# Performance work log

Hardware: AMD Instinct MI355X
Metric: run time of the kernel (lower is better)

The kernel has to match this reference:

```python
import jax, jax.numpy as jnp
import numpy as np

NUM_EMBEDDINGS = 1024
EMBEDDING_DIM = 256
COMMITMENT_COST = 0.25


def setup_inputs() -> dict:
    key = jax.random.key(0)
    k1, k2 = jax.random.split(key)
    inputs = jax.random.normal(k1, (32, EMBEDDING_DIM, 32, 32), dtype=jnp.float32)
    # torch init: uniform_(-1/K, 1/K)
    emb_w = jax.random.uniform(k2, (NUM_EMBEDDINGS, EMBEDDING_DIM), dtype=jnp.float32,
                               minval=-1.0 / NUM_EMBEDDINGS, maxval=1.0 / NUM_EMBEDDINGS)
    return {"inputs": inputs, "emb_w": emb_w}


def reference(inputs, emb_w):
    sg = jax.lax.stop_gradient
    # BCHW -> BHWC
    x = jnp.transpose(inputs, (0, 2, 3, 1))
    in_shape = x.shape
    flat = x.reshape(-1, EMBEDDING_DIM)  # [N, D]
    # squared L2 distances to codebook: [N, K]
    distances = (jnp.sum(flat * flat, axis=1, keepdims=True)
                 + jnp.sum(emb_w * emb_w, axis=1)
                 - 2.0 * jnp.matmul(flat, emb_w.T))
    idx = jnp.argmin(distances, axis=1)  # [N]
    encodings = jax.nn.one_hot(idx, NUM_EMBEDDINGS, dtype=jnp.float32)  # [N, K]
    # one-hot @ codebook == gather
    quantized = jnp.take(emb_w, idx, axis=0).reshape(in_shape)  # [B,H,W,D]
    e_latent_loss = jnp.mean((sg(quantized) - x) ** 2)
    q_latent_loss = jnp.mean((quantized - sg(x)) ** 2)
    loss = q_latent_loss + COMMITMENT_COST * e_latent_loss
    # straight-through estimator
    quantized_st = x + sg(quantized - x)
    avg_probs = jnp.mean(encodings, axis=0)
    perplexity = jnp.exp(-jnp.sum(avg_probs * jnp.log(avg_probs + 1e-10)))
    return (loss, jnp.transpose(quantized_st, (0, 3, 1, 2)), perplexity, encodings)
```

## Files before the change

kernel.cpp:

```cpp
#include <hip/hip_runtime.h>
#include <hip/hip_bf16.h>

typedef short short8 __attribute__((ext_vector_type(8)));
typedef float f32x4 __attribute__((ext_vector_type(4)));
typedef unsigned short u16x4 __attribute__((ext_vector_type(4)));

#define D_ 256
#define K_ 1024
#define HW_ 1024
#define NROWS_ 32768
#define QELEMS 8388608
#define NBLK_ (NROWS_ / 64)

static __device__ __forceinline__ unsigned short to_bf16(float v) {
    __hip_bfloat16 h = __float2bfloat16(v);
    return *(unsigned short*)&h;
}

__global__ __launch_bounds__(256) void vq_prep(const float* __restrict__ emb,
    unsigned short* __restrict__ ebf, float* __restrict__ enorm,
    int* __restrict__ counts, double* __restrict__ loss_acc, int* __restrict__ done)
{
    int k = blockIdx.x, t = threadIdx.x;
    float v = emb[k * D_ + t];
    ebf[k * D_ + t] = to_bf16(v);
    float s = v * v;
    for (int o = 32; o > 0; o >>= 1) s += __shfl_down(s, o);
    __shared__ float ws4[4];
    if ((t & 63) == 0) ws4[t >> 6] = s;
    __syncthreads();
    if (t == 0) enorm[k] = ws4[0] + ws4[1] + ws4[2] + ws4[3];
    if (k < 4) counts[k * 256 + t] = 0;
    if (k == 0 && t == 0) { *loss_acc = 0.0; *done = 0; }
}

__global__ __launch_bounds__(512, 4) void vq_main(
    const float* __restrict__ x, const float* __restrict__ emb,
    const unsigned short* __restrict__ ebf, const float* __restrict__ enorm,
    int* __restrict__ counts, double* __restrict__ loss_acc, int* __restrict__ done,
    float* __restrict__ out)
{
    __shared__ char smem[66560];
    __shared__ float xn[64][33];
    __shared__ float rminv[64][4];
    __shared__ int   rmini[64][4];
    __shared__ int   bestsh[64];
    __shared__ double sred2[8];
    __shared__ int lastflag;

    unsigned short* xs = (unsigned short*)smem;
    char* es = smem;

    const int t = threadIdx.x;
    const int n0 = blockIdx.x * 64;
    const int b = n0 >> 10;
    const int hw0 = n0 & 1023;
    const float* xbase = x + (size_t)b * (D_ * HW_) + hw0;

    {
        const int rt = t & 15;
        const int dg = t >> 4;
        const int r0 = rt * 4;
        float xp[4] = {0.f, 0.f, 0.f, 0.f};
#pragma unroll
        for (int m = 0; m < 2; ++m) {
            int d0 = (dg + 32 * m) * 4;
            f32x4 c[4];
#pragma unroll
            for (int q = 0; q < 4; ++q)
                c[q] = *(const f32x4*)(xbase + (size_t)(d0 + q) * HW_ + r0);
#pragma unroll
            for (int i = 0; i < 4; ++i) {
                u16x4 pk;
                pk[0] = to_bf16(c[0][i]); pk[1] = to_bf16(c[1][i]);
                pk[2] = to_bf16(c[2][i]); pk[3] = to_bf16(c[3][i]);
                xp[i] = fmaf(c[0][i], c[0][i], xp[i]);
                xp[i] = fmaf(c[1][i], c[1][i], xp[i]);
                xp[i] = fmaf(c[2][i], c[2][i], xp[i]);
                xp[i] = fmaf(c[3][i], c[3][i], xp[i]);
                int r = r0 + i;
                int byte = (r * 512 + d0 * 2) ^ ((r & 7) << 4);
                *(u16x4*)((char*)xs + byte) = pk;
            }
        }
#pragma unroll
        for (int i = 0; i < 4; ++i) xn[r0 + i][dg] = xp[i];
    }
    __syncthreads();

    const int lane = t & 63;
    const int w = t >> 6;
    const int rh = w & 1;
    const int cq = w >> 1;
    const int col = lane & 15;
    const int kg = lane >> 4;
    const char* ebf_bytes = (const char*)ebf;
    const int wbyte = w * 4096;

    {
#pragma unroll
        for (int j = 0; j < 4; ++j) {
            int p = wbyte + j * 1024 + lane * 16;
            int qq = p ^ (((p >> 9) & 7) << 4);
            __builtin_amdgcn_global_load_lds(ebf_bytes + qq, es + 32768 + wbyte + j * 1024, 16, 0, 0);
        }
    }

    short8 areg[2][8];
#pragma unroll
    for (int rt = 0; rt < 2; ++rt) {
        int row = rh * 32 + rt * 16 + col;
        int rowb = row * 512;
        int sw = (row & 7) << 4;
#pragma unroll
        for (int dc = 0; dc < 8; ++dc) {
            int byte = (rowb + dc * 64 + kg * 16) ^ sw;
            areg[rt][dc] = *(const short8*)((const char*)xs + byte);
        }
    }

    float v1[8]; int i1[8];
#pragma unroll
    for (int s = 0; s < 8; ++s) { v1[s] = 3.4e38f; i1[s] = 0x7fffffff; }

    float2* ezw = (float2*)(out + 8388610 + (size_t)(n0 + w * 8) * 1024);
    const float2 zz2 = {0.f, 0.f};

    for (int cc = 0; cc < 16; ++cc) {
        __syncthreads();
        const int hc = ((cc & 1) ^ 1) * 32768;
        if (cc < 15) {
            const char* src = ebf_bytes + (size_t)(cc + 1) * 32768;
            const int hn = (cc & 1) * 32768;
#pragma unroll
            for (int j = 0; j < 4; ++j) {
                int p = wbyte + j * 1024 + lane * 16;
                int qq = p ^ (((p >> 9) & 7) << 4);
                __builtin_amdgcn_global_load_lds(src + qq, es + hn + wbyte + j * 1024, 16, 0, 0);
            }
        }
        {
            float2* ez = ezw + cc * 256;
#pragma unroll
            for (int j = 0; j < 4; ++j) ez[j * 64 + lane] = zz2;
        }
        const int c0 = cq * 16 + col;
        const int sw0 = (c0 & 7) << 4;
        f32x4 acc0 = {0.f, 0.f, 0.f, 0.f};
        f32x4 acc1 = {0.f, 0.f, 0.f, 0.f};
#pragma unroll
        for (int dc = 0; dc < 8; ++dc) {
            short8 bf = *(const short8*)(es + hc + ((c0 * 512 + dc * 64 + kg * 16) ^ sw0));
            acc0 = __builtin_amdgcn_mfma_f32_16x16x32_bf16(areg[0][dc], bf, acc0, 0, 0, 0);
            acc1 = __builtin_amdgcn_mfma_f32_16x16x32_bf16(areg[1][dc], bf, acc1, 0, 0, 0);
        }
        int code = cc * 64 + c0;
        float bn = enorm[code];
#pragma unroll
        for (int r = 0; r < 4; ++r) {
            float dv = fmaf(-2.f, acc0[r], bn);
            if (dv < v1[r]) { v1[r] = dv; i1[r] = code; }
            float dw = fmaf(-2.f, acc1[r], bn);
            if (dw < v1[4 + r]) { v1[4 + r] = dw; i1[4 + r] = code; }
        }
    }

#pragma unroll
    for (int mask = 1; mask < 16; mask <<= 1) {
#pragma unroll
        for (int s = 0; s < 8; ++s) {
            float ov = __shfl_xor(v1[s], mask);
            int oi = __shfl_xor(i1[s], mask);
            if (ov < v1[s] || (ov == v1[s] && oi < i1[s])) { v1[s] = ov; i1[s] = oi; }
        }
    }
    if (col == 0) {
#pragma unroll
        for (int s = 0; s < 8; ++s) {
            int rt = s >> 2, r = s & 3;
            int row = rh * 32 + rt * 16 + kg * 4 + r;
            rminv[row][cq] = v1[s];
            rmini[row][cq] = i1[s];
        }
    }
    __syncthreads();

    if (t < 64) {
        float dmin = rminv[t][0]; int best = rmini[t][0];
#pragma unroll
        for (int g = 1; g < 4; ++g) {
            float cv = rminv[t][g]; int ci = rmini[t][g];
            if (cv < dmin || (cv == dmin && ci < best)) { dmin = cv; best = ci; }
        }
        bestsh[t] = best;
        atomicAdd(&counts[best], 1);
        float s = 0.f;
#pragma unroll 8
        for (int g = 0; g < 32; ++g) s += xn[t][g];
        float lrow = dmin + s;
        for (int o = 32; o > 0; o >>= 1) lrow += __shfl_down(lrow, o);
        if (t == 0) atomicAdd(loss_acc, (double)lrow);
    }
    __syncthreads();

    {
        int r = w * 8 + (lane & 7);
        int c = lane >> 3;
        const f32x4* src4 = (const f32x4*)emb + (size_t)bestsh[r] * 64 + c * 8;
        f32x4* dst4 = (f32x4*)smem + r * 65 + c * 8;
#pragma unroll
        for (int j = 0; j < 8; ++j) dst4[j] = src4[j];
    }
    __syncthreads();

    {
        const int hwr = t & 63;
        const int dq = t >> 6;
        float* outq = out + 1 + (size_t)b * (D_ * HW_) + hw0 + hwr;
        const float* qrow = (const float*)smem + hwr * 260;
#pragma unroll
        for (int dd = 0; dd < 32; ++dd) {
            int d = dq + dd * 8;
            outq[(size_t)d * HW_] = qrow[d];
        }
    }
    if (t < 64) out[8388610 + (size_t)(n0 + t) * 1024 + bestsh[t]] = 1.0f;
    __syncthreads();

    if (t == 0) {
        __threadfence();
        int old = atomicAdd(done, 1);
        lastflag = (old == NBLK_ - 1) ? 1 : 0;
    }
    __syncthreads();
    if (lastflag) {
        double s = 0.0;
#pragma unroll
        for (int j = 0; j < 2; ++j) {
            int k = t * 2 + j;
            int cnt = __hip_atomic_load(&counts[k], __ATOMIC_RELAXED, __HIP_MEMORY_SCOPE_AGENT);
            double p = (double)cnt / 32768.0;
            s += p * log(p + 1e-10);
        }
        for (int o = 32; o > 0; o >>= 1) s += __shfl_down(s, o);
        if (lane == 0) sred2[w] = s;
        __syncthreads();
        if (t == 0) {
            double tot = 0.0;
#pragma unroll
            for (int g = 0; g < 8; ++g) tot += sred2[g];
            double lw = __hip_atomic_load(loss_acc, __ATOMIC_RELAXED, __HIP_MEMORY_SCOPE_AGENT);
            out[0] = (float)(1.25 * lw / (double)QELEMS);
            out[8388609] = (float)exp(-tot);
        }
    }
}

extern "C" void kernel_launch(void* const* d_in, const int* in_sizes, int n_in,
                              void* d_out, int out_size, void* d_ws, size_t ws_size,
                              hipStream_t stream)
{
    const float* x = (const float*)d_in[0];
    const float* emb = (const float*)d_in[1];
    char* ws = (char*)d_ws;
    unsigned short* ebf = (unsigned short*)(ws);
    float* enorm = (float*)(ws + 524288);
    int* counts = (int*)(ws + 528384);
    double* lacc = (double*)(ws + 532480);
    int* done = (int*)(ws + 532488);
    float* out = (float*)d_out;

    vq_prep<<<K_, 256, 0, stream>>>(emb, ebf, enorm, counts, lacc, done);
    vq_main<<<NBLK_, 512, 0, stream>>>(x, emb, ebf, enorm, counts, lacc, done, out);
}
```

Baseline: 76.73 us.

## Cut LDS footprint, stage codebook norms in LDS, relax loop barrier waits

Shrinks shared memory by pre-reducing the per-row x-norm partials with shuffles (xn shrinks from 33 to 9 columns) and by swapping the padded quantized staging buffer for an XOR-swizzled one. This lets more blocks fit per CU under the 4-block launch bound. Codebook norms are copied once into LDS instead of being read from global memory on every chunk. The per-chunk __syncthreads is replaced by a partial vmcnt wait plus s_barrier, so the one-hot zero-fill stores can stay in flight, and the last chunk's zero stores are hoisted ahead of the loop. The vmcnt(4) count assumes a particular ordering of outstanding global loads and stores, which risks being subtly wrong.

```diff
diff --git a/kernel.cpp b/kernel.cpp
--- a/kernel.cpp
+++ b/kernel.cpp
@@ -40,8 +40,9 @@
     int* __restrict__ counts, double* __restrict__ loss_acc, int* __restrict__ done,
     float* __restrict__ out)
 {
-    __shared__ char smem[66560];
-    __shared__ float xn[64][33];
+    __shared__ char smem[65536];
+    __shared__ float xn[64][9];
+    __shared__ float ens[1024];
     __shared__ float rminv[64][4];
     __shared__ int   rmini[64][4];
     __shared__ int   bestsh[64];
@@ -57,10 +58,13 @@
     const int hw0 = n0 & 1023;
     const float* xbase = x + (size_t)b * (D_ * HW_) + hw0;
 
+    ens[t] = enorm[t];
+    ens[t + 512] = enorm[t + 512];
+
     {
         const int rt = t & 15;
+        const int r0 = rt * 4;
         const int dg = t >> 4;
-        const int r0 = rt * 4;
         float xp[4] = {0.f, 0.f, 0.f, 0.f};
 #pragma unroll
         for (int m = 0; m < 2; ++m) {
@@ -84,7 +88,15 @@
             }
         }
 #pragma unroll
-        for (int i = 0; i < 4; ++i) xn[r0 + i][dg] = xp[i];
+        for (int i = 0; i < 4; ++i) {
+            xp[i] += __shfl_down(xp[i], 32);
+            xp[i] += __shfl_down(xp[i], 16);
+        }
+        if ((t & 48) == 0) {
+            int w0 = t >> 6;
+#pragma unroll
+            for (int i = 0; i < 4; ++i) xn[r0 + i][w0] = xp[i];
+        }
     }
     __syncthreads();
 
@@ -97,6 +109,9 @@
     const char* ebf_bytes = (const char*)ebf;
     const int wbyte = w * 4096;
 
+    float2* ezw = (float2*)(out + 8388610 + (size_t)(n0 + w * 8) * 1024);
+    const float2 zz2 = {0.f, 0.f};
+
     {
 #pragma unroll
         for (int j = 0; j < 4; ++j) {
@@ -104,6 +119,11 @@
             int qq = p ^ (((p >> 9) & 7) << 4);
             __builtin_amdgcn_global_load_lds(ebf_bytes + qq, es + 32768 + wbyte + j * 1024, 16, 0, 0);
         }
+        __builtin_amdgcn_sched_barrier(0);
+        float2* ez = ezw + 15 * 256;
+#pragma unroll
+        for (int j = 0; j < 4; ++j) ez[j * 64 + lane] = zz2;
+        __builtin_amdgcn_sched_barrier(0);
     }
 
     short8 areg[2][8];
@@ -123,11 +143,10 @@
 #pragma unroll
     for (int s = 0; s < 8; ++s) { v1[s] = 3.4e38f; i1[s] = 0x7fffffff; }
 
-    float2* ezw = (float2*)(out + 8388610 + (size_t)(n0 + w * 8) * 1024);
-    const float2 zz2 = {0.f, 0.f};
-
     for (int cc = 0; cc < 16; ++cc) {
-        __syncthreads();
+        asm volatile("s_waitcnt vmcnt(4)" ::: "memory");
+        __builtin_amdgcn_s_barrier();
+        __builtin_amdgcn_sched_barrier(0);
         const int hc = ((cc & 1) ^ 1) * 32768;
         if (cc < 15) {
             const char* src = ebf_bytes + (size_t)(cc + 1) * 32768;
@@ -138,11 +157,11 @@
                 int qq = p ^ (((p >> 9) & 7) << 4);
                 __builtin_amdgcn_global_load_lds(src + qq, es + hn + wbyte + j * 1024, 16, 0, 0);
             }
-        }
-        {
+            __builtin_amdgcn_sched_barrier(0);
             float2* ez = ezw + cc * 256;
 #pragma unroll
             for (int j = 0; j < 4; ++j) ez[j * 64 + lane] = zz2;
+            __builtin_amdgcn_sched_barrier(0);
         }
         const int c0 = cq * 16 + col;
         const int sw0 = (c0 & 7) << 4;
@@ -155,7 +174,7 @@
             acc1 = __builtin_amdgcn_mfma_f32_16x16x32_bf16(areg[1][dc], bf, acc1, 0, 0, 0);
         }
         int code = cc * 64 + c0;
-        float bn = enorm[code];
+        float bn = ens[code];
 #pragma unroll
         for (int r = 0; r < 4; ++r) {
             float dv = fmaf(-2.f, acc0[r], bn);
@@ -195,8 +214,8 @@
         bestsh[t] = best;
         atomicAdd(&counts[best], 1);
         float s = 0.f;
-#pragma unroll 8
-        for (int g = 0; g < 32; ++g) s += xn[t][g];
+#pragma unroll
+        for (int g = 0; g < 8; ++g) s += xn[t][g];
         float lrow = dmin + s;
         for (int o = 32; o > 0; o >>= 1) lrow += __shfl_down(lrow, o);
         if (t == 0) atomicAdd(loss_acc, (double)lrow);
@@ -204,12 +223,21 @@
     __syncthreads();
 
     {
-        int r = w * 8 + (lane & 7);
-        int c = lane >> 3;
-        const f32x4* src4 = (const f32x4*)emb + (size_t)bestsh[r] * 64 + c * 8;
-        f32x4* dst4 = (f32x4*)smem + r * 65 + c * 8;
-#pragma unroll
-        for (int j = 0; j < 8; ++j) dst4[j] = src4[j];
+        int rr = lane >> 3;
+        int r  = w * 8 + rr;
+        int c  = lane & 7;
+        const f32x4* src4 = (const f32x4*)emb + (size_t)bestsh[r] * 64;
+        float* q = (float*)smem + r * 256;
+        int xr = r & 31;
+#pragma unroll
+        for (int j = 0; j < 8; ++j) {
+            f32x4 v = src4[8 * j + c];
+#pragma unroll
+            for (int k = 0; k < 4; ++k) {
+                int d = 4 * (8 * j + c) + k;
+                q[d ^ xr] = v[k];
+            }
+        }
     }
     __syncthreads();
 
@@ -217,11 +245,12 @@
         const int hwr = t & 63;
         const int dq = t >> 6;
         float* outq = out + 1 + (size_t)b * (D_ * HW_) + hw0 + hwr;
-        const float* qrow = (const float*)smem + hwr * 260;
+        const float* q = (const float*)smem + hwr * 256;
+        int xr = hwr & 31;
 #pragma unroll
         for (int dd = 0; dd < 32; ++dd) {
             int d = dq + dd * 8;
-            outq[(size_t)d * HW_] = qrow[d];
+            outq[(size_t)d * HW_] = q[d ^ xr];
         }
     }
     if (t < 64) out[8388610 + (size_t)(n0 + t) * 1024 + bestsh[t]] = 1.0f;
```

After: 74.93 us. -2.3%, faster.
